# Kernel optimization log

Hardware: AMD Instinct MI355X
Metric: run time of the kernel (lower is better)

The kernel has to match this reference:

```python
import jax, jax.numpy as jnp
import numpy as np

DIM = 768
HEADS = 12
HEAD_DIM = DIM // HEADS
SCALE = HEAD_DIM ** (-0.5)


def setup_inputs() -> dict:
    key = jax.random.key(0)
    k1, k2, k3 = jax.random.split(key, 3)
    x = jax.random.normal(k1, (4, 2048, DIM), dtype=jnp.float32)
    # nn.Linear(dim, 3*dim, bias=False): weight [3*dim, dim]
    w_qkv = jax.random.normal(k2, (3 * DIM, DIM), dtype=jnp.float32) * (DIM ** -0.5)
    # nn.Linear(dim, dim) with bias
    w_proj = jax.random.normal(k3, (DIM, DIM), dtype=jnp.float32) * (DIM ** -0.5)
    b_proj = jnp.zeros((DIM,), dtype=jnp.float32)
    return {"x": x, "w_qkv": w_qkv, "w_proj": w_proj, "b_proj": b_proj}


def reference(x, w_qkv, w_proj, b_proj):
    B, N, C = x.shape
    H, D = HEADS, HEAD_DIM
    qkv = jnp.einsum('bnc,oc->bno', x, w_qkv)  # [B,N,3C]
    qkv = qkv.reshape(B, N, 3, H, D).transpose(2, 0, 3, 1, 4)  # [3,B,H,N,D]
    q, k, v = qkv[0], qkv[1], qkv[2]
    attn = jnp.einsum('bhnd,bhmd->bhnm', q, k) * SCALE  # [B,H,N,N]
    attn = jax.nn.softmax(attn, axis=-1)
    attn = jax.nn.softmax(attn, axis=-1)  # double softmax, as in original
    out = jnp.einsum('bhnm,bhmd->bhnd', attn, v)  # [B,H,N,D]
    out = out.transpose(0, 2, 1, 3).reshape(B, N, C)
    return jnp.einsum('bnc,oc->bno', out, w_proj) + b_proj
```

## Files before the change

kernel.cpp:

```cpp
#include <hip/hip_runtime.h>
#include <hip/hip_bf16.h>

#define DIM 768
#define HEADS 12
#define HD 64
#define SEQ 2048
#define BATCH 4
#define BHN 48
#define TOK 8192

#if __has_builtin(__builtin_amdgcn_exp2f)
#define EXP2F __builtin_amdgcn_exp2f
#else
#define EXP2F exp2f
#endif
#define EXP_C 0.1803368801111244f

using short8  = __attribute__((ext_vector_type(8))) short;
using short4v = __attribute__((ext_vector_type(4))) short;
using float4v = __attribute__((ext_vector_type(4))) float;

__device__ __forceinline__ short f2b(float f) {
    union { float f; unsigned u; } v; v.f = f;
    unsigned r = v.u + 0x7FFF + ((v.u >> 16) & 1);
    return (short)(r >> 16);
}
__device__ __forceinline__ float b2f(short s) {
    union { unsigned u; float f; } v;
    v.u = ((unsigned)(unsigned short)s) << 16;
    return v.f;
}
__device__ __forceinline__ unsigned pk2(float a, float b) {
    union { float f; unsigned u; } x, y; x.f = a; y.f = b;
    return __builtin_amdgcn_perm(x.u + 0x8000u, y.u + 0x8000u, 0x03020706u);
}

typedef const __attribute__((address_space(1))) unsigned GU;
typedef __attribute__((address_space(3))) unsigned LU;
__device__ __forceinline__ void gload_lds16(const short* g, short* l) {
    __builtin_amdgcn_global_load_lds((GU*)g, (LU*)l, 16, 0, 0);
}

__global__ void cast_all(const float* __restrict__ x, const float* __restrict__ wq,
                         const float* __restrict__ wp,
                         short* __restrict__ xb, short* __restrict__ wqb,
                         short* __restrict__ wpb, int nx4, int nq4) {
    int i = blockIdx.x * 256 + threadIdx.x;
    const float* in; short* out; int j = i;
    if (i < nx4)            { in = x;  out = xb;  }
    else if (i < nx4 + nq4) { in = wq; out = wqb; j = i - nx4; }
    else                    { in = wp; out = wpb; j = i - nx4 - nq4; }
    float4 f = ((const float4*)in)[j];
    short4 o;
    o.x = f2b(f.x); o.y = f2b(f.y); o.z = f2b(f.z); o.w = f2b(f.w);
    ((short4*)out)[j] = o;
}

__global__ void vsum_kernel(const short* __restrict__ Vw, float* __restrict__ Vsum) {
    int wid  = blockIdx.x * 4 + (threadIdx.x >> 6);
    int lane = threadIdx.x & 63;
    int bh = wid >> 6, d = wid & 63;
    const short* base = Vw + (size_t)bh * (SEQ * 64) + d * 128;
    float s = 0.f;
    for (int i = lane; i < SEQ; i += 64)
        s += b2f(base[(i >> 7) * 8192 + (i & 127)]);
    #pragma unroll
    for (int m = 1; m < 64; m <<= 1) s += __shfl_xor(s, m, 64);
    if (lane == 0) Vsum[wid] = s;
}

__global__ __launch_bounds__(256, 4)
void gemm_qkv(const short* __restrict__ A, const short* __restrict__ Bw,
              short* __restrict__ Qw, short* __restrict__ Kw, short* __restrict__ Vw)
{
    __shared__ __align__(16) short As[2][128 * 32];
    __shared__ __align__(16) short Bs[2][128 * 32];

    const int tid  = threadIdx.x;
    const int lane = tid & 63;
    const int wave = tid >> 6;
    const int wm = (wave >> 1) * 64, wn = (wave & 1) * 64;
    const int l15 = lane & 15, quad = lane >> 4;

    const int gid = blockIdx.x;
    const int w   = gid >> 3;
    const int ybl = (gid & 7) * 8 + (w & 7);
    const int xbl = w >> 3;

    const bool vpart = (xbl >= 12);
    const short* rowsP = vpart ? (Bw + 1536 * 768) : A;
    const short* colsP = vpart ? A : Bw;
    const int m0 = vpart ? (xbl - 12) * 128 : ybl * 128;
    const int n0 = vpart ? ybl * 128 : xbl * 128;
    const int K = DIM;

    float4v acc[4][4];
    #pragma unroll
    for (int i = 0; i < 4; i++)
        #pragma unroll
        for (int j = 0; j < 4; j++)
            acc[i][j] = (float4v){0.f, 0.f, 0.f, 0.f};

    const int G0 = wave * 128 + lane;
    const int G1 = G0 + 64;
    const int rA0 = G0 >> 2, cA0 = (G0 & 3) * 8;
    const int rA1 = G1 >> 2, cA1 = (G1 & 3) * 8;
    const int ldsoff = wave * 1024;

    for (int kt = 0; kt < K; kt += 64) {
        #pragma unroll
        for (int s = 0; s < 2; s++) {
            const int kc = kt + s * 32;
            gload_lds16(&rowsP[(size_t)(m0 + rA0) * K + kc + cA0], &As[s][ldsoff]);
            gload_lds16(&rowsP[(size_t)(m0 + rA1) * K + kc + cA1], &As[s][ldsoff + 512]);
            gload_lds16(&colsP[(size_t)(n0 + rA0) * K + kc + cA0], &Bs[s][ldsoff]);
            gload_lds16(&colsP[(size_t)(n0 + rA1) * K + kc + cA1], &Bs[s][ldsoff + 512]);
        }
        __syncthreads();
        #pragma unroll
        for (int s = 0; s < 2; s++) {
            short8 af[4], bfr[4];
            #pragma unroll
            for (int t = 0; t < 4; t++) {
                af[t]  = *(const short8*)&As[s][(wm + t * 16 + l15) * 32 + quad * 8];
                bfr[t] = *(const short8*)&Bs[s][(wn + t * 16 + l15) * 32 + quad * 8];
            }
            #pragma unroll
            for (int tm = 0; tm < 4; tm++)
                #pragma unroll
                for (int tn = 0; tn < 4; tn++)
                    acc[tm][tn] = __builtin_amdgcn_mfma_f32_16x16x32_bf16(af[tm], bfr[tn], acc[tm][tn], 0, 0, 0);
        }
        __syncthreads();
    }

    #pragma unroll
    for (int tm = 0; tm < 4; tm++)
        #pragma unroll
        for (int tn = 0; tn < 4; tn++)
            #pragma unroll
            for (int r = 0; r < 4; r++) {
                int row = m0 + wm + tm * 16 + quad * 4 + r;
                int col = n0 + wn + tn * 16 + l15;
                float v = acc[tm][tn][r];
                if (vpart) {
                    int hh = row >> 6, d = row & 63;
                    int b = col >> 11, n = col & 2047;
                    int bh = b * HEADS + hh;
                    int t = n >> 7;
                    int c2 = (n >> 5) & 3, wk = n & 31;
                    int slot = ((wk & 15) >> 2) * 8 + ((wk & 16) >> 2) + (wk & 3);
                    int g  = c2 * 4 + (slot >> 3);
                    int gp = g ^ (d & 7);
                    Vw[(size_t)bh * (SEQ * 64) + t * 8192 + d * 128 + gp * 8 + (slot & 7)] = f2b(v);
                } else {
                    int hh = (col & 767) >> 6, d = col & 63;
                    int b = row >> 11, n = row & 2047;
                    int bh = b * HEADS + hh;
                    int t = n >> 7, r7 = n & 127;
                    size_t idx = (size_t)bh * (SEQ * 64) + t * 8192 + r7 * 64
                               + (((d >> 3) ^ (r7 & 7)) << 3) + (d & 7);
                    if (col < 768) Qw[idx] = f2b(v * EXP_C);
                    else           Kw[idx] = f2b(v);
                }
            }
}

__global__ __launch_bounds__(256, 4)
void gemm_proj(const short* __restrict__ A, const short* __restrict__ Bw,
               const float* __restrict__ bias, float* __restrict__ Out)
{
    __shared__ __align__(16) short As[2][128 * 32];
    __shared__ __align__(16) short Bs[2][64 * 32];

    const int tid  = threadIdx.x;
    const int lane = tid & 63;
    const int wave = tid >> 6;
    const int wm = (wave >> 1) * 64, wn = (wave & 1) * 32;
    const int l15 = lane & 15, quad = lane >> 4;

    const int gid = blockIdx.x;
    const int w   = gid >> 3;
    const int ybl = (gid & 7) * 8 + (w & 7);
    const int xbl = w >> 3;
    const int m0 = ybl * 128, n0 = xbl * 64;
    const int K = DIM;

    float4v acc[4][2];
    #pragma unroll
    for (int i = 0; i < 4; i++)
        #pragma unroll
        for (int j = 0; j < 2; j++)
            acc[i][j] = (float4v){0.f, 0.f, 0.f, 0.f};

    const int GA0 = wave * 128 + lane, GA1 = GA0 + 64;
    const int rA0 = GA0 >> 2, cA0 = (GA0 & 3) * 8;
    const int rA1 = GA1 >> 2, cA1 = (GA1 & 3) * 8;
    const int GB0 = wave * 64 + lane;
    const int rB0 = GB0 >> 2, cB0 = (GB0 & 3) * 8;
    const int ldsoffA = wave * 1024, ldsoffB = wave * 512;

    for (int kt = 0; kt < K; kt += 64) {
        #pragma unroll
        for (int s = 0; s < 2; s++) {
            const int kc = kt + s * 32;
            gload_lds16(&A [(size_t)(m0 + rA0) * K + kc + cA0], &As[s][ldsoffA]);
            gload_lds16(&A [(size_t)(m0 + rA1) * K + kc + cA1], &As[s][ldsoffA + 512]);
            gload_lds16(&Bw[(size_t)(n0 + rB0) * K + kc + cB0], &Bs[s][ldsoffB]);
        }
        __syncthreads();
        #pragma unroll
        for (int s = 0; s < 2; s++) {
            short8 af[4], bfr[2];
            #pragma unroll
            for (int t = 0; t < 4; t++)
                af[t] = *(const short8*)&As[s][(wm + t * 16 + l15) * 32 + quad * 8];
            #pragma unroll
            for (int t = 0; t < 2; t++)
                bfr[t] = *(const short8*)&Bs[s][(wn + t * 16 + l15) * 32 + quad * 8];
            #pragma unroll
            for (int tm = 0; tm < 4; tm++)
                #pragma unroll
                for (int tn = 0; tn < 2; tn++)
                    acc[tm][tn] = __builtin_amdgcn_mfma_f32_16x16x32_bf16(af[tm], bfr[tn], acc[tm][tn], 0, 0, 0);
        }
        __syncthreads();
    }

    #pragma unroll
    for (int tm = 0; tm < 4; tm++)
        #pragma unroll
        for (int tn = 0; tn < 2; tn++)
            #pragma unroll
            for (int r = 0; r < 4; r++) {
                int row = m0 + wm + tm * 16 + quad * 4 + r;
                int col = n0 + wn + tn * 16 + l15;
                Out[(size_t)row * 768 + col] = acc[tm][tn][r] + bias[col];
            }
}

__global__ __launch_bounds__(256, 4)
void attn_kernel(const short* __restrict__ Qw, const short* __restrict__ Kw,
                 const short* __restrict__ Vw, const float* __restrict__ Vsum,
                 short* __restrict__ Ow)
{
    __shared__ __align__(16) short KE[8192];
    __shared__ __align__(16) short VT[8192];

    const int tid  = threadIdx.x;
    const int lane = tid & 63, wave = tid >> 6;
    const int l15 = lane & 15, quad = lane >> 4;
    const int r7  = l15 & 7;
    const int bid = blockIdx.x;
    const int ii  = bid >> 3;
    const int bh  = (bid & 7) * 6 + (ii >> 4);
    const int qt  = ii & 15;
    const int wq  = wave * 32;

    const short* Qp = Qw + (size_t)bh * (SEQ * 64) + qt * 8192;
    const short* Kp = Kw + (size_t)bh * (SEQ * 64);
    const short* Vp = Vw + (size_t)bh * (SEQ * 64);

    short8 onesf;
    #pragma unroll
    for (int j = 0; j < 8; j++) onesf[j] = (l15 == 0) ? (short)0x3F80 : (short)0;

    const int sg = wave * 4;

    #pragma unroll
    for (int h = 0; h < 4; h++)
        gload_lds16(&Qp[(sg + h) * 512 + lane * 8], &KE[(sg + h) * 512]);
    __syncthreads();
    short8 aq[2][2];
    #pragma unroll
    for (int nb = 0; nb < 2; nb++)
        #pragma unroll
        for (int kk = 0; kk < 2; kk++) {
            int r = wq + nb * 16 + l15;
            aq[nb][kk] = *(const short8*)&KE[r * 64 + (((kk * 4 + quad) ^ r7) << 3)];
        }

    float4v Aacc[2][4], Lacc[2];
    #pragma unroll
    for (int mb = 0; mb < 2; mb++) {
        Lacc[mb] = (float4v){0.f, 0.f, 0.f, 0.f};
        #pragma unroll
        for (int t = 0; t < 4; t++) Aacc[mb][t] = (float4v){0.f, 0.f, 0.f, 0.f};
    }

    for (int kt = 0; kt < 16; kt++) {
        __syncthreads();
        #pragma unroll
        for (int h = 0; h < 4; h++) {
            gload_lds16(&Kp[kt * 8192 + (sg + h) * 512 + lane * 8], &KE[(sg + h) * 512]);
            gload_lds16(&Vp[kt * 8192 + (sg + h) * 512 + lane * 8], &VT[(sg + h) * 512]);
        }
        __syncthreads();

        #pragma unroll
        for (int c2 = 0; c2 < 4; c2++) {
            union AE { unsigned u[4]; short8 s; };
            AE ae[2];
            #pragma unroll
            for (int tn2 = 0; tn2 < 2; tn2++) {
                const int tn = c2 * 2 + tn2;
                const int base = (tn * 16 + l15) * 64;
                short8 b0 = *(const short8*)&KE[base + ((quad ^ r7) << 3)];
                short8 b1 = *(const short8*)&KE[base + (((4 + quad) ^ r7) << 3)];
                #pragma unroll
                for (int nb = 0; nb < 2; nb++) {
                    float4v s = (float4v){0.f, 0.f, 0.f, 0.f};
                    s = __builtin_amdgcn_mfma_f32_16x16x32_bf16(b0, aq[nb][0], s, 0, 0, 0);
                    s = __builtin_amdgcn_mfma_f32_16x16x32_bf16(b1, aq[nb][1], s, 0, 0, 0);
                    ae[nb].u[tn2 * 2]     = pk2(EXP2F(s[0]), EXP2F(s[1]));
                    ae[nb].u[tn2 * 2 + 1] = pk2(EXP2F(s[2]), EXP2F(s[3]));
                }
            }
            __builtin_amdgcn_s_setprio(1);
            Lacc[0] = __builtin_amdgcn_mfma_f32_16x16x32_bf16(ae[0].s, onesf, Lacc[0], 0, 0, 0);
            Lacc[1] = __builtin_amdgcn_mfma_f32_16x16x32_bf16(ae[1].s, onesf, Lacc[1], 0, 0, 0);
            #pragma unroll
            for (int tn = 0; tn < 4; tn++) {
                const int d = tn * 16 + l15;
                short8 bv = *(const short8*)&VT[d * 128 + (((c2 * 4 + quad) ^ r7) << 3)];
                Aacc[0][tn] = __builtin_amdgcn_mfma_f32_16x16x32_bf16(ae[0].s, bv, Aacc[0][tn], 0, 0, 0);
                Aacc[1][tn] = __builtin_amdgcn_mfma_f32_16x16x32_bf16(ae[1].s, bv, Aacc[1][tn], 0, 0, 0);
            }
            __builtin_amdgcn_s_setprio(0);
        }
    }

    const int b = bh / HEADS, hh = bh - (bh / HEADS) * HEADS;
    #pragma unroll
    for (int mb = 0; mb < 2; mb++)
        #pragma unroll
        for (int r = 0; r < 4; r++) {
            float il = 1.f / __shfl(Lacc[mb][r], lane & 48, 64);
            int row = qt * 128 + wq + mb * 16 + quad * 4 + r;
            int tok = b * SEQ + row;
            #pragma unroll
            for (int tn = 0; tn < 4; tn++) {
                int d = tn * 16 + l15;
                float vs = Vsum[bh * 64 + d];
                float val = (vs + Aacc[mb][tn][r] * il) * (1.f / 2049.f);
                Ow[(size_t)tok * 768 + hh * 64 + d] = f2b(val);
            }
        }
}

extern "C" void kernel_launch(void* const* d_in, const int* in_sizes, int n_in,
                              void* d_out, int out_size, void* d_ws, size_t ws_size,
                              hipStream_t stream) {
    const float* x      = (const float*)d_in[0];
    const float* w_qkv  = (const float*)d_in[1];
    const float* w_proj = (const float*)d_in[2];
    const float* b_proj = (const float*)d_in[3];
    float* out = (float*)d_out;

    char* ws = (char*)d_ws;
    size_t off = 0;
    auto alloc = [&](size_t bytes) {
        void* p = ws + off;
        off += (bytes + 255) & ~(size_t)255;
        return p;
    };
    short* x_bf  = (short*)alloc((size_t)TOK * DIM * 2);
    short* wq_bf = (short*)alloc((size_t)3 * DIM * DIM * 2);
    short* wp_bf = (short*)alloc((size_t)DIM * DIM * 2);
    short* Qw    = (short*)alloc((size_t)BHN * SEQ * 64 * 2);
    short* Kw    = (short*)alloc((size_t)BHN * SEQ * 64 * 2);
    short* Vw    = (short*)alloc((size_t)BHN * SEQ * 64 * 2);
    short* Ow    = (short*)alloc((size_t)TOK * DIM * 2);
    float* Vsum  = (float*)alloc((size_t)BHN * 64 * 4);

    int nx4 = TOK * DIM / 4, nq4 = 3 * DIM * DIM / 4, np4 = DIM * DIM / 4;
    int tot4 = nx4 + nq4 + np4;
    cast_all<<<tot4 / 256, 256, 0, stream>>>(x, w_qkv, w_proj, x_bf, wq_bf, wp_bf, nx4, nq4);

    gemm_qkv<<<1152, 256, 0, stream>>>(x_bf, wq_bf, Qw, Kw, Vw);

    vsum_kernel<<<BHN * 64 / 4, 256, 0, stream>>>(Vw, Vsum);

    attn_kernel<<<BHN * 16, 256, 0, stream>>>(Qw, Kw, Vw, Vsum, Ow);

    gemm_proj<<<768, 256, 0, stream>>>(Ow, wp_bf, b_proj, out);
}
```

Baseline: 208.6 us.

## Double-buffer K/V tiles in attention with 64-key stages and async prefetch

Re-tiles the K/V layout written by the QKV GEMM and read by vsum into 64-key chunks, and makes the attention kernel double-buffer them. The tile for step kt+2 is prefetched with direct-to-LDS loads while the current tile is computed, using explicit vmcnt waits and barriers. This hides the global-load latency that the old load-then-sync loop exposed on each of its 16 iterations. The trade-off is twice as many iterations and barriers, plus hand-managed waitcnt logic that must match the number of outstanding loads.

```diff
diff --git a/kernel.cpp b/kernel.cpp
--- a/kernel.cpp
+++ b/kernel.cpp
@@ -60,10 +60,10 @@
     int wid  = blockIdx.x * 4 + (threadIdx.x >> 6);
     int lane = threadIdx.x & 63;
     int bh = wid >> 6, d = wid & 63;
-    const short* base = Vw + (size_t)bh * (SEQ * 64) + d * 128;
+    const short* base = Vw + (size_t)bh * (SEQ * 64) + d * 64;
     float s = 0.f;
     for (int i = lane; i < SEQ; i += 64)
-        s += b2f(base[(i >> 7) * 8192 + (i & 127)]);
+        s += b2f(base[(i >> 6) * 4096 + (i & 63)]);
     #pragma unroll
     for (int m = 1; m < 64; m <<= 1) s += __shfl_xor(s, m, 64);
     if (lane == 0) Vsum[wid] = s;
@@ -147,19 +147,17 @@
                     int hh = row >> 6, d = row & 63;
                     int b = col >> 11, n = col & 2047;
                     int bh = b * HEADS + hh;
-                    int t = n >> 7;
-                    int c2 = (n >> 5) & 3, wk = n & 31;
+                    int t2 = n >> 6, c2h = (n >> 5) & 1, wk = n & 31;
                     int slot = ((wk & 15) >> 2) * 8 + ((wk & 16) >> 2) + (wk & 3);
-                    int g  = c2 * 4 + (slot >> 3);
-                    int gp = g ^ (d & 7);
-                    Vw[(size_t)bh * (SEQ * 64) + t * 8192 + d * 128 + gp * 8 + (slot & 7)] = f2b(v);
+                    int g2 = c2h * 4 + (slot >> 3);
+                    int gp2 = g2 ^ (d & 7);
+                    Vw[(size_t)bh * (SEQ * 64) + t2 * 4096 + d * 64 + gp2 * 8 + (slot & 7)] = f2b(v);
                 } else {
                     int hh = (col & 767) >> 6, d = col & 63;
                     int b = row >> 11, n = row & 2047;
                     int bh = b * HEADS + hh;
-                    int t = n >> 7, r7 = n & 127;
-                    size_t idx = (size_t)bh * (SEQ * 64) + t * 8192 + r7 * 64
-                               + (((d >> 3) ^ (r7 & 7)) << 3) + (d & 7);
+                    size_t idx = (size_t)bh * (SEQ * 64) + (size_t)n * 64
+                               + (((d >> 3) ^ (n & 7)) << 3) + (d & 7);
                     if (col < 768) Qw[idx] = f2b(v * EXP_C);
                     else           Kw[idx] = f2b(v);
                 }
@@ -244,8 +242,7 @@
                  const short* __restrict__ Vw, const float* __restrict__ Vsum,
                  short* __restrict__ Ow)
 {
-    __shared__ __align__(16) short KE[8192];
-    __shared__ __align__(16) short VT[8192];
+    __shared__ __align__(16) short LDS[16384];
 
     const int tid  = threadIdx.x;
     const int lane = tid & 63, wave = tid >> 6;
@@ -265,11 +262,11 @@
     #pragma unroll
     for (int j = 0; j < 8; j++) onesf[j] = (l15 == 0) ? (short)0x3F80 : (short)0;
 
-    const int sg = wave * 4;
-
-    #pragma unroll
-    for (int h = 0; h < 4; h++)
-        gload_lds16(&Qp[(sg + h) * 512 + lane * 8], &KE[(sg + h) * 512]);
+    #pragma unroll
+    for (int h = 0; h < 4; h++) {
+        const int g = wave * 4 + h;
+        gload_lds16(&Qp[g * 512 + lane * 8], &LDS[g * 512]);
+    }
     __syncthreads();
     short8 aq[2][2];
     #pragma unroll
@@ -277,8 +274,9 @@
         #pragma unroll
         for (int kk = 0; kk < 2; kk++) {
             int r = wq + nb * 16 + l15;
-            aq[nb][kk] = *(const short8*)&KE[r * 64 + (((kk * 4 + quad) ^ r7) << 3)];
-        }
+            aq[nb][kk] = *(const short8*)&LDS[r * 64 + (((kk * 4 + quad) ^ r7) << 3)];
+        }
+    __syncthreads();
 
     float4v Aacc[2][4], Lacc[2];
     #pragma unroll
@@ -288,25 +286,40 @@
         for (int t = 0; t < 4; t++) Aacc[mb][t] = (float4v){0.f, 0.f, 0.f, 0.f};
     }
 
-    for (int kt = 0; kt < 16; kt++) {
-        __syncthreads();
-        #pragma unroll
-        for (int h = 0; h < 4; h++) {
-            gload_lds16(&Kp[kt * 8192 + (sg + h) * 512 + lane * 8], &KE[(sg + h) * 512]);
-            gload_lds16(&Vp[kt * 8192 + (sg + h) * 512 + lane * 8], &VT[(sg + h) * 512]);
-        }
-        __syncthreads();
-
-        #pragma unroll
-        for (int c2 = 0; c2 < 4; c2++) {
+    auto STAGE = [&](int t2, int kbuf) {
+        const int kb = kbuf * 4096;
+        #pragma unroll
+        for (int h = 0; h < 2; h++) {
+            const int g = wave * 2 + h;
+            gload_lds16(&Kp[(size_t)t2 * 4096 + g * 512 + lane * 8], &LDS[kb + g * 512]);
+            gload_lds16(&Vp[(size_t)t2 * 4096 + g * 512 + lane * 8], &LDS[8192 + kb + g * 512]);
+        }
+    };
+
+    STAGE(0, 0);
+    STAGE(1, 1);
+
+    for (int kt = 0; kt < 32; kt++) {
+        if (kt < 31) { asm volatile("s_waitcnt vmcnt(4)" ::: "memory"); }
+        else         { asm volatile("s_waitcnt vmcnt(0)" ::: "memory"); }
+        __builtin_amdgcn_sched_barrier(0);
+        __builtin_amdgcn_s_barrier();
+        __builtin_amdgcn_sched_barrier(0);
+
+        const int kb = (kt & 1) * 4096;
+        const short* KB = &LDS[kb];
+        const short* VB = &LDS[8192 + kb];
+
+        #pragma unroll
+        for (int c2 = 0; c2 < 2; c2++) {
             union AE { unsigned u[4]; short8 s; };
             AE ae[2];
             #pragma unroll
             for (int tn2 = 0; tn2 < 2; tn2++) {
-                const int tn = c2 * 2 + tn2;
-                const int base = (tn * 16 + l15) * 64;
-                short8 b0 = *(const short8*)&KE[base + ((quad ^ r7) << 3)];
-                short8 b1 = *(const short8*)&KE[base + (((4 + quad) ^ r7) << 3)];
+                const int row = (c2 * 2 + tn2) * 16 + l15;
+                const short* rp = &KB[row * 64];
+                short8 b0 = *(const short8*)&rp[(quad ^ r7) << 3];
+                short8 b1 = *(const short8*)&rp[((4 + quad) ^ r7) << 3];
                 #pragma unroll
                 for (int nb = 0; nb < 2; nb++) {
                     float4v s = (float4v){0.f, 0.f, 0.f, 0.f};
@@ -322,12 +335,17 @@
             #pragma unroll
             for (int tn = 0; tn < 4; tn++) {
                 const int d = tn * 16 + l15;
-                short8 bv = *(const short8*)&VT[d * 128 + (((c2 * 4 + quad) ^ r7) << 3)];
+                short8 bv = *(const short8*)&VB[d * 64 + (((c2 * 4 + quad) ^ r7) << 3)];
                 Aacc[0][tn] = __builtin_amdgcn_mfma_f32_16x16x32_bf16(ae[0].s, bv, Aacc[0][tn], 0, 0, 0);
                 Aacc[1][tn] = __builtin_amdgcn_mfma_f32_16x16x32_bf16(ae[1].s, bv, Aacc[1][tn], 0, 0, 0);
             }
             __builtin_amdgcn_s_setprio(0);
         }
+
+        __builtin_amdgcn_sched_barrier(0);
+        __builtin_amdgcn_s_barrier();
+        __builtin_amdgcn_sched_barrier(0);
+        if (kt < 30) STAGE(kt + 2, kt & 1);
     }
 
     const int b = bh / HEADS, hh = bh - (bh / HEADS) * HEADS;
```

Result: no change. 206.0 us (-1.3%).
